# Kernel tuning notes

Hardware: AMD Instinct MI355X
Metric: run time of the kernel (lower is better)

Reference implementation:

```python
import jax, jax.numpy as jnp
import numpy as np

N, E, B, M = 50000, 100000, 50, 50
NPG = N // B            # atoms per graph
DIN, H1, H2, DE, AAF, G = 32, 32, 64, 16, 95, 128
K, T = 3, 6             # ARMA num_stacks, num_layers
F1, F2, F3 = 64, 32, 16
EA = 2 * (M - 1)        # amino-acid edges per graph


def setup_inputs() -> dict:
    key = jax.random.key(0)
    ks = jax.random.split(key, 24)
    s = 0.05
    def w(k, shape):
        return jax.random.normal(k, shape, jnp.float32) * s
    return {
        "x": jax.random.normal(ks[0], (N, DIN), jnp.float32),
        "edge_attr": jax.random.normal(ks[1], (E, DE), jnp.float32),
        "aa_features": jax.random.normal(ks[2], (B, M, AAF), jnp.float32),
        "edge_index": jax.random.randint(ks[3], (2, E), 0, N),
        "monomer_labels": jax.random.randint(ks[4], (B, NPG), 0, M),
        "amino_edge_index": jax.random.randint(ks[5], (2, EA), 0, M),
        "W_e1": w(ks[6], (DE, DIN * H1)), "b_e1": jnp.zeros((DIN * H1,), jnp.float32),
        "root1": w(ks[7], (DIN, H1)), "bias1": jnp.zeros((H1,), jnp.float32),
        "W_e2": w(ks[8], (DE, H1 * H2)), "b_e2": jnp.zeros((H1 * H2,), jnp.float32),
        "root2": w(ks[9], (H1, H2)), "bias2": jnp.zeros((H2,), jnp.float32),
        "Wa_atom": w(ks[10], (H2, 1)), "ba_atom": jnp.zeros((1,), jnp.float32),
        "arma_init_w": w(ks[11], (K, H2 + AAF, G)),
        "arma_w": w(ks[12], (T - 1, K, G, G)),
        "arma_root_w": w(ks[13], (T, K, H2 + AAF, G)),
        "arma_bias": jnp.zeros((T, K, G), jnp.float32),
        "Wa_aa": w(ks[14], (G, 1)), "ba_aa": jnp.zeros((1,), jnp.float32),
        "W1": w(ks[15], (G, F1)), "b1": jnp.zeros((F1,), jnp.float32),
        "W2": w(ks[16], (F1, F2)), "b2": jnp.zeros((F2,), jnp.float32),
        "W3": w(ks[17], (F2, F3)), "b3": jnp.zeros((F3,), jnp.float32),
        "W4": w(ks[18], (F3, 1)), "b4": jnp.zeros((1,), jnp.float32),
    }


def _nnconv(h, src, dst, edge_attr, Wm, bm, root, bias, fin, fout):
    # NNConv (aggr='add'): edge MLP -> per-edge weight matrix, gather-matmul-scatter
    w_e = (edge_attr @ Wm + bm).reshape(-1, fin, fout)            # [E, fin, fout]
    msg = jnp.einsum('ef,efo->eo', h[src], w_e)                   # [E, fout]
    agg = jax.ops.segment_sum(msg, dst, num_segments=h.shape[0])  # scatter-add to targets
    return agg + h @ root + bias


def _forward(x, edge_attr, aa_features, W_e1, b_e1, root1, bias1, W_e2, b_e2, root2, bias2,
             Wa_atom, ba_atom, arma_init_w, arma_w, arma_root_w, arma_bias, Wa_aa, ba_aa,
             W1, b1, W2, b2, W3, b3, W4, b4, edge_index, monomer_labels, amino_edge_index):
    src, dst = edge_index[0], edge_index[1]
    h = jax.nn.relu(_nnconv(x, src, dst, edge_attr, W_e1, b_e1, root1, bias1, DIN, H1))
    h = jax.nn.relu(_nnconv(h, src, dst, edge_attr, W_e2, b_e2, root2, bias2, H1, H2))

    # per-graph attention readout over atoms -> amino-acid embeddings (scatter by monomer label)
    xg = h.reshape(B, NPG, H2)
    attn = jax.nn.softmax(xg @ Wa_atom + ba_atom, axis=1)         # softmax over atoms in graph
    wx = xg * attn
    aa = jax.vmap(lambda wxi, lbl: jax.ops.segment_sum(wxi, lbl, num_segments=M))(wx, monomer_labels)
    h_aa = jnp.concatenate([aa, aa_features], axis=-1)            # [B, M, H2+95]

    # ARMAConv: gcn_norm without self-loops on amino-acid graph (shared across graphs)
    asrc, adst = amino_edge_index[0], amino_edge_index[1]
    deg = jax.ops.segment_sum(jnp.ones((EA,), x.dtype), adst, num_segments=M)
    dinv = jnp.where(deg > 0, 1.0 / jnp.sqrt(jnp.maximum(deg, 1.0)), 0.0)
    norm = dinv[asrc] * dinv[adst]                                # [EA]

    def arma(x0):  # x0: [M, H2+95]
        out = jnp.einsum('mf,kfo->kmo', x0, arma_init_w)          # [K, M, G]
        for t in range(T):
            if t > 0:
                out = jnp.einsum('kmo,kop->kmp', out, arma_w[t - 1])
            msg = out[:, asrc] * norm[None, :, None]              # [K, EA, G]
            prop = jax.vmap(lambda m: jax.ops.segment_sum(m, adst, num_segments=M))(msg)
            rootc = jnp.einsum('mf,kfo->kmo', x0, arma_root_w[t])
            out = jax.nn.relu(prop + rootc + arma_bias[t][:, None, :])
        return out.mean(axis=0)                                   # mean over stacks -> [M, G]

    g = jax.vmap(arma)(h_aa)                                      # [B, M, G]

    # attention readout over amino acids
    attn2 = jax.nn.softmax(g @ Wa_aa + ba_aa, axis=1)
    p = jnp.sum(g * attn2, axis=1)                                # [B, G]

    p = jax.nn.relu(p @ W1 + b1)
    p = jax.nn.relu(p @ W2 + b2)
    p = jax.nn.relu(p @ W3 + b3)
    p = p @ W4 + b4
    return p.reshape(-1)                                          # [B]


def reference(x, edge_attr, aa_features, edge_index, monomer_labels, amino_edge_index,
              W_e1, b_e1, root1, bias1, W_e2, b_e2, root2, bias2, Wa_atom, ba_atom,
              arma_init_w, arma_w, arma_root_w, arma_bias, Wa_aa, ba_aa,
              W1, b1, W2, b2, W3, b3, W4, b4):
    return _forward(x, edge_attr, aa_features, W_e1, b_e1, root1, bias1, W_e2, b_e2, root2, bias2,
                    Wa_atom, ba_atom, arma_init_w, arma_w, arma_root_w, arma_bias, Wa_aa, ba_aa,
                    W1, b1, W2, b2, W3, b3, W4, b4, edge_index, monomer_labels, amino_edge_index)
```

## Files before the change

kernel.cpp:

```cpp
#include <hip/hip_runtime.h>
#include <math.h>

#define N_ATOMS 50000
#define E_EDGES 100000
#define B_G     50
#define M_M     50
#define NPG     1000
#define DIN     32
#define H1C     32
#define H2C     64
#define DEC     16
#define AAF     95
#define G_DIM   128
#define K_ST    3
#define T_L     6
#define EA_E    98
#define XDIM    159
#define NS      21
#define MPAD    64
#define GP      132
#define GPS     136
#define KP2     168
#define KW      544
#define SLC     10
#define APB     100
#define NSB     ((N_ATOMS + 255) / 256)

#define OFF_WE2 (H1C * KW)
#define OFF_WT  (OFF_WE2 + H2C * KW)
#define OFF_AW  (OFF_WT + NS * XDIM * G_DIM)
#define OFF_DEG (OFF_AW + (T_L - 1) * K_ST * G_DIM * G_DIM)
#define PREP_TOTAL (OFF_DEG + E_EDGES)

typedef __attribute__((ext_vector_type(8))) short bf16x8;
typedef __attribute__((ext_vector_type(4))) float f32x4;
typedef __attribute__((ext_vector_type(4))) unsigned int u32x4;

__device__ __forceinline__ short f2bf(float f) {
    unsigned int u = __float_as_uint(f);
    unsigned int r = (u + 0x7FFFu + ((u >> 16) & 1u)) >> 16;
    return (short)r;
}
__device__ __forceinline__ float bf2f(short b) {
    return __uint_as_float(((unsigned int)(unsigned short)b) << 16);
}
__device__ __forceinline__ unsigned int cvtpk_bf16(float lo, float hi) {
    unsigned int r;
    asm("v_cvt_pk_bf16_f32 %0, %1, %2" : "=v"(r) : "v"(lo), "v"(hi));
    return r;
}

__device__ __forceinline__ void f4fma(float4& d, float s, const float4& v) {
    d.x += s * v.x; d.y += s * v.y; d.z += s * v.z; d.w += s * v.w;
}
__device__ __forceinline__ void f4add(float4& d, const float4& v) {
    d.x += v.x; d.y += v.y; d.z += v.z; d.w += v.w;
}
__device__ __forceinline__ void f4relu(float4& d) {
    d.x = fmaxf(d.x, 0.f); d.y = fmaxf(d.y, 0.f);
    d.z = fmaxf(d.z, 0.f); d.w = fmaxf(d.w, 0.f);
}

__global__ __launch_bounds__(256) void prep_all(
    const float* __restrict__ We1, const float* __restrict__ be1, short* __restrict__ WB1,
    const float* __restrict__ We2, const float* __restrict__ be2, short* __restrict__ WB2,
    const float* __restrict__ init_w, const float* __restrict__ root_w, short* __restrict__ Wtb,
    const float* __restrict__ arma_w, short* __restrict__ Wab,
    const int* __restrict__ eidx, int* __restrict__ deg,
    const int* __restrict__ aei, int* __restrict__ aa_off,
    int* __restrict__ aa_src, float* __restrict__ aa_nrm)
{
    int tid = threadIdx.x;
    if (blockIdx.x == 0) {
        __shared__ int   sdeg[M_M];
        __shared__ int   scur[M_M];
        __shared__ float sdinv[M_M];
        __shared__ int   soff[M_M + 1];
        if (tid < M_M) { sdeg[tid] = 0; scur[tid] = 0; }
        __syncthreads();
        if (tid < EA_E) atomicAdd(&sdeg[aei[EA_E + tid]], 1);
        __syncthreads();
        if (tid < M_M) {
            float dv = (float)sdeg[tid];
            sdinv[tid] = (dv > 0.f) ? (1.f / sqrtf(fmaxf(dv, 1.f))) : 0.f;
        }
        __syncthreads();
        if (tid == 0) {
            soff[0] = 0;
            for (int m = 0; m < M_M; ++m) soff[m + 1] = soff[m] + sdeg[m];
        }
        __syncthreads();
        if (tid < EA_E) {
            int ss = aei[tid], dd = aei[EA_E + tid];
            int pos = atomicAdd(&scur[dd], 1);
            int idx = soff[dd] + pos;
            aa_src[idx] = ss;
            aa_nrm[idx] = sdinv[ss] * sdinv[dd];
        }
        if (tid < M_M + 1) aa_off[tid] = soff[tid];
        return;
    }
    int idx = (blockIdx.x - 1) * 256 + tid;
    if (idx < OFF_WE2) {
        int o = idx / KW, k = idx - o * KW;
        float v = (k < 512) ? We1[(size_t)k * H1C + o]
                            : be1[(size_t)(k - 512) * H1C + o];
        WB1[idx] = f2bf(v);
    } else if (idx < OFF_WT) {
        int rem = idx - OFF_WE2;
        int o = rem / KW, k = rem - o * KW;
        float v = (k < 512) ? We2[(size_t)k * H2C + o]
                            : be2[(size_t)(k - 512) * H2C + o];
        WB2[rem] = f2bf(v);
    } else if (idx < OFF_AW) {
        int rem = idx - OFF_WT;
        int s = rem / (XDIM * G_DIM);
        int r2 = rem - s * XDIM * G_DIM;
        int k = r2 / G_DIM, n = r2 - k * G_DIM;
        float v = (s < K_ST) ? init_w[rem]
                             : root_w[(size_t)(s - K_ST) * XDIM * G_DIM + r2];
        Wtb[(size_t)s * G_DIM * KP2 + n * KP2 + k] = f2bf(v);
    } else if (idx < OFF_DEG) {
        int rem = idx - OFF_AW;
        int slot = rem / (G_DIM * G_DIM);
        int r2 = rem - slot * G_DIM * G_DIM;
        int p = r2 / G_DIM, n = r2 - p * G_DIM;
        Wab[(size_t)slot * G_DIM * G_DIM + n * G_DIM + p] = f2bf(arma_w[rem]);
    } else if (idx < PREP_TOTAL) {
        int e = idx - OFF_DEG;
        atomicAdd(&deg[eidx[E_EDGES + e]], 1);
    }
}

__global__ __launch_bounds__(256) void scan_part(const int* __restrict__ deg,
                                                 int* __restrict__ bsum)
{
    __shared__ int tmp[256];
    int tid = threadIdx.x;
    int n = blockIdx.x * 256 + tid;
    tmp[tid] = (n < N_ATOMS) ? deg[n] : 0;
    __syncthreads();
    for (int off = 128; off > 0; off >>= 1) {
        if (tid < off) tmp[tid] += tmp[tid + off];
        __syncthreads();
    }
    if (tid == 0) bsum[blockIdx.x] = tmp[0];
}

__global__ __launch_bounds__(256) void scan_mid(const int* __restrict__ bsum,
                                                int* __restrict__ bpre)
{
    __shared__ int tmp[256];
    int tid = threadIdx.x;
    int v = (tid < NSB) ? bsum[tid] : 0;
    tmp[tid] = v;
    __syncthreads();
    for (int off = 1; off < 256; off <<= 1) {
        int t = tmp[tid];
        int add = (tid >= off) ? tmp[tid - off] : 0;
        __syncthreads();
        tmp[tid] = t + add;
        __syncthreads();
    }
    if (tid < NSB) bpre[tid] = tmp[tid] - v;
}

__global__ __launch_bounds__(256) void scan_out(int* __restrict__ deg_off,
                                                const int* __restrict__ bpre)
{
    __shared__ int tmp[256];
    int tid = threadIdx.x;
    int n = blockIdx.x * 256 + tid;
    int v = (n < N_ATOMS) ? deg_off[n] : 0;
    tmp[tid] = v;
    __syncthreads();
    for (int off = 1; off < 256; off <<= 1) {
        int t = tmp[tid];
        int add = (tid >= off) ? tmp[tid - off] : 0;
        __syncthreads();
        tmp[tid] = t + add;
        __syncthreads();
    }
    int incl = tmp[tid];
    int base = bpre[blockIdx.x];
    if (n < N_ATOMS) deg_off[n] = base + incl - v;
    if (n == N_ATOMS - 1) deg_off[N_ATOMS] = base + incl;
}

template<int FOUT, int NTT, int WGRP, int MTB, bool CIPOS>
__global__ __launch_bounds__(256) void edge_msg_v2(
    const float* __restrict__ h, const float* __restrict__ ea,
    const int* __restrict__ eidx, int* __restrict__ ipos,
    const int* __restrict__ off, int* __restrict__ cursor,
    const short* __restrict__ WB, float* __restrict__ msg)
{
    constexpr int KS = 17;
    __shared__ int iplds[MTB * 16];
    int tid  = threadIdx.x;
    int lane = tid & 63, wave = tid >> 6;
    int l16  = lane & 15, quad = lane >> 4;
    int nt   = wave % NTT, tg = wave / NTT;
    int ebase = blockIdx.x * (MTB * 16);

    if (CIPOS) {
        if (tid < MTB * 16) {
            int e = ebase + tid;
            if (e < E_EDGES) {
                int d = eidx[E_EDGES + e];
                int pos = atomicAdd(&cursor[d], 1);
                int p = off[d] + pos;
                iplds[tid] = p;
                ipos[e] = p;
            }
        }
    }

    bf16x8 Bfr[KS];
    {
        const short* wb = WB + (size_t)(nt * 16 + l16) * KW;
        #pragma unroll
        for (int ks = 0; ks < KS; ++ks)
            Bfr[ks] = *(const bf16x8*)(wb + ks * 32 + quad * 8);
    }
    if (CIPOS) __syncthreads();

    for (int t = tg; t < MTB; t += WGRP) {
        int e  = ebase + t * 16 + l16;
        int es = (e < E_EDGES) ? e : (E_EDGES - 1);
        int s  = eidx[es];
        float4 h0 = *(const float4*)(h + (size_t)s * 32 + quad * 8);
        float4 h1 = *(const float4*)(h + (size_t)s * 32 + quad * 8 + 4);
        float hf[8] = {h0.x, h0.y, h0.z, h0.w, h1.x, h1.y, h1.z, h1.w};
        float4 e0 = *(const float4*)(ea + (size_t)es * DEC);
        float4 e1 = *(const float4*)(ea + (size_t)es * DEC + 4);
        float4 e2 = *(const float4*)(ea + (size_t)es * DEC + 8);
        float4 e3 = *(const float4*)(ea + (size_t)es * DEC + 12);
        float eaf[16] = {e0.x, e0.y, e0.z, e0.w, e1.x, e1.y, e1.z, e1.w,
                         e2.x, e2.y, e2.z, e2.w, e3.x, e3.y, e3.z, e3.w};

        f32x4 acc = (f32x4){0.f, 0.f, 0.f, 0.f};
        #pragma unroll
        for (int ks = 0; ks < KS; ++ks) {
            u32x4 av;
            if (ks < DEC) {
                float fac = eaf[ks];
                #pragma unroll
                for (int j = 0; j < 4; ++j)
                    av[j] = cvtpk_bf16(fac * hf[2 * j], fac * hf[2 * j + 1]);
            } else {
                #pragma unroll
                for (int j = 0; j < 4; ++j)
                    av[j] = cvtpk_bf16(hf[2 * j], hf[2 * j + 1]);
            }
            bf16x8 a = __builtin_bit_cast(bf16x8, av);
            acc = __builtin_amdgcn_mfma_f32_16x16x32_bf16(a, Bfr[ks], acc, 0, 0, 0);
        }
        int erb = ebase + t * 16 + quad * 4;
        #pragma unroll
        for (int r = 0; r < 4; ++r) {
            int ee = erb + r;
            if (ee < E_EDGES) {
                int p = CIPOS ? iplds[t * 16 + quad * 4 + r] : ipos[ee];
                msg[(size_t)p * FOUT + nt * 16 + l16] = acc[r];
            }
        }
    }
}

template<int FIN, int FOUT, bool SCORE>
__global__ __launch_bounds__(256) void gather_update(
    const float* __restrict__ msg, const int* __restrict__ off,
    const float* __restrict__ hin,
    const float* __restrict__ root, const float* __restrict__ bias,
    float* __restrict__ hout,
    const float* __restrict__ wa, const float* __restrict__ ba,
    float* __restrict__ sc)
{
    constexpr int NPB = 256 / FOUT;
    __shared__ float rlds[FIN][FOUT];
    __shared__ float hlds[NPB][FIN];
    int tid = threadIdx.x;
    for (int i = tid; i < FIN * FOUT / 4; i += 256) {
        *(float4*)&rlds[0][i * 4] = *(const float4*)(root + i * 4);
    }
    int nb = blockIdx.x * NPB;
    for (int i = tid; i < NPB * FIN; i += 256) {
        int ln = i / FIN, f = i % FIN;
        int n = nb + ln;
        hlds[ln][f] = (n < N_ATOMS) ? hin[(size_t)n * FIN + f] : 0.f;
    }
    __syncthreads();

    int ln = tid / FOUT, o = tid % FOUT;
    int n = nb + ln;
    if (n >= N_ATOMS) return;
    float acc = bias[o];
    #pragma unroll 8
    for (int f = 0; f < FIN; ++f) acc += hlds[ln][f] * rlds[f][o];
    int j0 = off[n], j1 = off[n + 1];
    for (int j = j0; j < j1; ++j) {
        acc += msg[(size_t)j * FOUT + o];
    }
    float hv = fmaxf(acc, 0.f);
    hout[(size_t)n * FOUT + o] = hv;
    if constexpr (SCORE) {
        static_assert(FOUT == 64, "score fusion needs node==wave");
        float sv = hv * wa[o];
        #pragma unroll
        for (int d = 32; d > 0; d >>= 1) sv += __shfl_down(sv, d);
        if (o == 0) sc[n] = sv + ba[0];
    }
}

__global__ __launch_bounds__(256) void atom_scatter_sm(
    const float* __restrict__ h2, const float* __restrict__ sc,
    const int* __restrict__ labels, float* __restrict__ partial)
{
    __shared__ float aa4[4][M_M][H2C];
    __shared__ float red[256];
    int b = blockIdx.x / SLC, s = blockIdx.x % SLC;
    int tid = threadIdx.x;
    int wave = tid >> 6, lane = tid & 63;
    const float* sb = sc + (size_t)b * NPG;

    for (int i = tid; i < 4 * M_M * H2C; i += 256) ((float*)aa4)[i] = 0.f;

    float lmax = -1e30f;
    for (int n = tid; n < NPG; n += 256) lmax = fmaxf(lmax, sb[n]);
    red[tid] = lmax;
    __syncthreads();
    for (int off = 128; off > 0; off >>= 1) {
        if (tid < off) red[tid] = fmaxf(red[tid], red[tid + off]);
        __syncthreads();
    }
    float mx = red[0];
    __syncthreads();
    float lsum = 0.f;
    for (int n = tid; n < NPG; n += 256) lsum += expf(sb[n] - mx);
    red[tid] = lsum;
    __syncthreads();
    for (int off = 128; off > 0; off >>= 1) {
        if (tid < off) red[tid] += red[tid + off];
        __syncthreads();
    }
    float inv = 1.f / red[0];
    __syncthreads();

    int nbase = s * APB;
    const float* hb = h2 + (size_t)b * NPG * H2C;
    #pragma unroll 5
    for (int it = 0; it < APB / 4; ++it) {
        int n = nbase + it * 4 + wave;
        int lbl = labels[b * NPG + n];
        float w = expf(sb[n] - mx) * inv;
        float hv = hb[(size_t)n * H2C + lane];
        aa4[wave][lbl][lane] += hv * w;
    }
    __syncthreads();
    float* pb = partial + (size_t)(b * SLC + s) * M_M * H2C;
    for (int i = tid; i < M_M * H2C; i += 256) {
        float v = ((float*)aa4)[i] + ((float*)aa4)[M_M * H2C + i]
                + ((float*)aa4)[2 * M_M * H2C + i] + ((float*)aa4)[3 * M_M * H2C + i];
        pb[i] = v;
    }
}

__global__ __launch_bounds__(256) void x0_finalize(
    const float* __restrict__ partial, const float* __restrict__ aaf,
    short* __restrict__ x0b)
{
    int idx = blockIdx.x * 256 + threadIdx.x;
    if (idx >= B_G * MPAD * KP2) return;
    int b = idx / (MPAD * KP2);
    int rem = idx - b * (MPAD * KP2);
    int m = rem / KP2, k = rem - m * KP2;
    float v = 0.f;
    if (m < M_M) {
        if (k < H2C) {
            const float* pb = partial + (size_t)b * SLC * M_M * H2C + m * H2C + k;
            #pragma unroll
            for (int s = 0; s < SLC; ++s) v += pb[(size_t)s * (M_M * H2C)];
        } else if (k < XDIM) {
            v = aaf[((size_t)b * M_M + m) * AAF + (k - H2C)];
        }
    }
    x0b[idx] = f2bf(v);
}

__global__ __launch_bounds__(256) void rc_gemm_mfma(
    const short* __restrict__ x0b, const short* __restrict__ Wtb,
    float* __restrict__ RC)
{
    int b = blockIdx.x / NS, s = blockIdx.x % NS;
    int tid = threadIdx.x;
    int lane = tid & 63, wave = tid >> 6;
    int l16 = lane & 15, quad = lane >> 4;
    const short* xa = x0b + (size_t)b * MPAD * KP2 + (wave * 16 + l16) * KP2;
    const short* wb = Wtb + (size_t)s * G_DIM * KP2;

    f32x4 acc[8];
    #pragma unroll
    for (int nt = 0; nt < 8; ++nt) acc[nt] = (f32x4){0.f, 0.f, 0.f, 0.f};

    #pragma unroll
    for (int ks = 0; ks < 5; ++ks) {
        bf16x8 a = *(const bf16x8*)(xa + ks * 32 + quad * 8);
        #pragma unroll
        for (int nt = 0; nt < 8; ++nt) {
            bf16x8 bf = *(const bf16x8*)(wb + (nt * 16 + l16) * KP2 + ks * 32 + quad * 8);
            acc[nt] = __builtin_amdgcn_mfma_f32_16x16x32_bf16(a, bf, acc[nt], 0, 0, 0);
        }
    }
    float* op = RC + (size_t)(b * NS + s) * M_M * G_DIM;
    #pragma unroll
    for (int nt = 0; nt < 8; ++nt) {
        #pragma unroll
        for (int r = 0; r < 4; ++r) {
            int m = wave * 16 + quad * 4 + r;
            if (m < M_M)
                op[m * G_DIM + nt * 16 + l16] = acc[nt][r];
        }
    }
}

__global__ __launch_bounds__(512) void arma_iter(
    const float* __restrict__ RC, const short* __restrict__ Wab,
    const float* __restrict__ arma_bias,
    const int* __restrict__ aa_off, const int* __restrict__ aa_src,
    const float* __restrict__ aa_nrm, float* __restrict__ gfull)
{
    __shared__ float Abuf[MPAD][GP];
    __shared__ float Bbuf[MPAD][GP];
    __shared__ short Bb16[MPAD][GPS];
    __shared__ int   s_off[M_M + 1];
    __shared__ int   s_src[EA_E];
    __shared__ float s_nrm[EA_E];
    int b = blockIdx.x / K_ST, k = blockIdx.x % K_ST;
    int tid = threadIdx.x;
    int oi = tid & 15, mi = tid >> 4;
    int c0 = oi * 4, c1 = 64 + oi * 4;
    int lane = tid & 63, wave = tid >> 6;
    int l16 = lane & 15, quad = lane >> 4;
    int mt = wave >> 1, nh = wave & 1;

    const float* rcb = RC + (size_t)b * NS * M_M * G_DIM;
    if (tid < M_M + 1) s_off[tid] = aa_off[tid];
    if (tid < EA_E) { s_src[tid] = aa_src[tid]; s_nrm[tid] = aa_nrm[tid]; }

    for (int i = tid; i < MPAD * G_DIM; i += 512) {
        int m = i >> 7, o = i & 127;
        Abuf[m][o] = (m < M_M) ? rcb[(size_t)k * M_M * G_DIM + i] : 0.f;
    }
    for (int i = tid; i < MPAD * GPS / 2; i += 512) {
        ((int*)Bb16)[i] = 0;
    }
    __syncthreads();

    for (int t = 0; t < T_L; ++t) {
        if (t > 0) {
            const short* aw = Wab + (size_t)((t - 1) * K_ST + k) * G_DIM * G_DIM;
            f32x4 acc[4];
            #pragma unroll
            for (int nt = 0; nt < 4; ++nt) acc[nt] = (f32x4){0.f, 0.f, 0.f, 0.f};
            #pragma unroll
            for (int ks = 0; ks < 4; ++ks) {
                bf16x8 a = *(const bf16x8*)&Bb16[mt * 16 + l16][ks * 32 + quad * 8];
                #pragma unroll
                for (int nt = 0; nt < 4; ++nt) {
                    int n0 = (nh * 4 + nt) * 16 + l16;
                    bf16x8 bf = *(const bf16x8*)(aw + n0 * G_DIM + ks * 32 + quad * 8);
                    acc[nt] = __builtin_amdgcn_mfma_f32_16x16x32_bf16(a, bf, acc[nt], 0, 0, 0);
                }
            }
            #pragma unroll
            for (int nt = 0; nt < 4; ++nt) {
                #pragma unroll
                for (int r = 0; r < 4; ++r) {
                    Abuf[mt * 16 + quad * 4 + r][(nh * 4 + nt) * 16 + l16] = acc[nt][r];
                }
            }
            __syncthreads();
        }
        const float* rct = rcb + (size_t)(K_ST + t * K_ST + k) * M_M * G_DIM;
        const float* bb  = arma_bias + ((size_t)t * K_ST + k) * G_DIM;
        float4 bias0 = *(const float4*)(bb + c0);
        float4 bias1 = *(const float4*)(bb + c1);
        #pragma unroll
        for (int r = 0; r < 2; ++r) {
            int m = mi * 2 + r;
            if (m < M_M) {
                const float* rr = rct + (size_t)m * G_DIM;
                float4 v0 = bias0, v1 = bias1;
                f4add(v0, *(const float4*)(rr + c0));
                f4add(v1, *(const float4*)(rr + c1));
                int j0 = s_off[m], j1 = s_off[m + 1];
                for (int j = j0; j < j1; ++j) {
                    float nv = s_nrm[j];
                    const float* ap = &Abuf[s_src[j]][0];
                    f4fma(v0, nv, *(const float4*)(ap + c0));
                    f4fma(v1, nv, *(const float4*)(ap + c1));
                }
                f4relu(v0);
                f4relu(v1);
                *(float4*)&Bbuf[m][c0] = v0;
                *(float4*)&Bbuf[m][c1] = v1;
                unsigned int p0 = cvtpk_bf16(v0.x, v0.y);
                unsigned int p1 = cvtpk_bf16(v0.z, v0.w);
                unsigned int p2 = cvtpk_bf16(v1.x, v1.y);
                unsigned int p3 = cvtpk_bf16(v1.z, v1.w);
                *(uint2*)&Bb16[m][c0] = make_uint2(p0, p1);
                *(uint2*)&Bb16[m][c1] = make_uint2(p2, p3);
            }
        }
        __syncthreads();
    }
    float* gb = gfull + ((size_t)(b * K_ST + k)) * M_M * G_DIM;
    for (int i = tid; i < M_M * G_DIM; i += 512) {
        int m = i >> 7, o = i & 127;
        gb[i] = Bbuf[m][o];
    }
}

__global__ __launch_bounds__(128) void aa_readout_mlp(
    const float* __restrict__ gfull, const float* __restrict__ wa,
    const float* __restrict__ ba,
    const float* __restrict__ W1, const float* __restrict__ b1,
    const float* __restrict__ W2, const float* __restrict__ b2,
    const float* __restrict__ W3, const float* __restrict__ b3,
    const float* __restrict__ W4, const float* __restrict__ b4,
    float* __restrict__ out)
{
    __shared__ float g[M_M][G_DIM + 1];
    __shared__ float s2[M_M];
    __shared__ float p[G_DIM];
    __shared__ float r1[64], r2[32], r3[16];
    int b = blockIdx.x, tid = threadIdx.x;
    const float* g0 = gfull + (size_t)b * K_ST * M_M * G_DIM;
    for (int i = tid; i < M_M * G_DIM; i += 128) {
        int m = i >> 7, o = i & 127;
        g[m][o] = (g0[i] + g0[M_M*G_DIM + i] + g0[2*M_M*G_DIM + i]) * (1.f/3.f);
    }
    __syncthreads();
    if (tid < M_M) {
        float sv = ba[0];
        for (int o = 0; o < G_DIM; ++o) sv += g[tid][o] * wa[o];
        s2[tid] = sv;
    }
    __syncthreads();
    if (tid == 0) {
        float mx = -1e30f;
        for (int m = 0; m < M_M; ++m) mx = fmaxf(mx, s2[m]);
        float den = 0.f;
        for (int m = 0; m < M_M; ++m) den += expf(s2[m] - mx);
        float inv = 1.f / den;
        for (int m = 0; m < M_M; ++m) s2[m] = expf(s2[m] - mx) * inv;
    }
    __syncthreads();
    {
        float pv = 0.f;
        for (int m = 0; m < M_M; ++m) pv += g[m][tid] * s2[m];
        p[tid] = pv;
    }
    __syncthreads();
    if (tid < 64) {
        float v = b1[tid];
        for (int i = 0; i < 128; ++i) v += p[i] * W1[i * 64 + tid];
        r1[tid] = fmaxf(v, 0.f);
    }
    __syncthreads();
    if (tid < 32) {
        float v = b2[tid];
        for (int i = 0; i < 64; ++i) v += r1[i] * W2[i * 32 + tid];
        r2[tid] = fmaxf(v, 0.f);
    }
    __syncthreads();
    if (tid < 16) {
        float v = b3[tid];
        for (int i = 0; i < 32; ++i) v += r2[i] * W3[i * 16 + tid];
        r3[tid] = fmaxf(v, 0.f);
    }
    __syncthreads();
    if (tid == 0) {
        float v = b4[0];
        for (int i = 0; i < 16; ++i) v += r3[i] * W4[i];
        out[b] = v;
    }
}

extern "C" void kernel_launch(void* const* d_in, const int* in_sizes, int n_in,
                              void* d_out, int out_size, void* d_ws, size_t ws_size,
                              hipStream_t stream)
{
    (void)in_sizes; (void)n_in; (void)out_size; (void)ws_size;
    const float* x            = (const float*)d_in[0];
    const float* edge_attr    = (const float*)d_in[1];
    const float* aa_features  = (const float*)d_in[2];
    const int*   edge_index   = (const int*)  d_in[3];
    const int*   mono_labels  = (const int*)  d_in[4];
    const int*   amino_ei     = (const int*)  d_in[5];
    const float* W_e1 = (const float*)d_in[6];
    const float* b_e1 = (const float*)d_in[7];
    const float* root1= (const float*)d_in[8];
    const float* bias1= (const float*)d_in[9];
    const float* W_e2 = (const float*)d_in[10];
    const float* b_e2 = (const float*)d_in[11];
    const float* root2= (const float*)d_in[12];
    const float* bias2= (const float*)d_in[13];
    const float* Wa_atom = (const float*)d_in[14];
    const float* ba_atom = (const float*)d_in[15];
    const float* arma_init_w = (const float*)d_in[16];
    const float* arma_w      = (const float*)d_in[17];
    const float* arma_root_w = (const float*)d_in[18];
    const float* arma_bias   = (const float*)d_in[19];
    const float* Wa_aa = (const float*)d_in[20];
    const float* ba_aa = (const float*)d_in[21];
    const float* W1 = (const float*)d_in[22];
    const float* b1 = (const float*)d_in[23];
    const float* W2 = (const float*)d_in[24];
    const float* b2 = (const float*)d_in[25];
    const float* W3 = (const float*)d_in[26];
    const float* b3 = (const float*)d_in[27];
    const float* W4 = (const float*)d_in[28];
    const float* b4 = (const float*)d_in[29];

    float* ws = (float*)d_ws;
    float* h1    = ws;
    float* h2    = h1   + (size_t)N_ATOMS * H1C;
    float* h_aa  = h2   + (size_t)N_ATOMS * H2C;
    float* sc    = h_aa + (size_t)B_G * M_M * XDIM;
    int*   aa_off = (int*)(sc + (size_t)B_G * NPG);
    int*   aa_src = aa_off + (M_M + 1);
    float* aa_nrm = (float*)(aa_src + EA_E);
    int*   deg_off = (int*)(aa_nrm + EA_E);
    int*   cursor  = deg_off + (N_ATOMS + 1);
    int*   ipos    = cursor + N_ATOMS;
    int*   bsum    = ipos + E_EDGES;
    int*   bpre    = bsum + 256;
    float* RC    = (float*)(bpre + 256);
    float* gfull = RC + (size_t)B_G * NS * M_M * G_DIM;
    short* Wtb   = (short*)((((uintptr_t)(gfull + (size_t)B_G * K_ST * M_M * G_DIM)) + 15)
                            & ~(uintptr_t)15);
    short* x0b   = Wtb + (size_t)NS * G_DIM * KP2;
    short* Wab   = x0b + (size_t)B_G * MPAD * KP2;
    short* WB1   = Wab + (size_t)(T_L - 1) * K_ST * G_DIM * G_DIM;
    short* WB2   = WB1 + (size_t)H1C * KW;
    float* msg   = RC;
    float* partial = RC;
    (void)h_aa;

    (void)hipMemsetAsync(deg_off, 0, (2 * N_ATOMS + 1) * sizeof(int), stream);

    prep_all<<<1 + (PREP_TOTAL + 255) / 256, 256, 0, stream>>>(
        W_e1, b_e1, WB1, W_e2, b_e2, WB2,
        arma_init_w, arma_root_w, Wtb, arma_w, Wab,
        edge_index, deg_off, amino_ei, aa_off, aa_src, aa_nrm);

    scan_part<<<NSB, 256, 0, stream>>>(deg_off, bsum);
    scan_mid<<<1, 256, 0, stream>>>(bsum, bpre);
    scan_out<<<NSB, 256, 0, stream>>>(deg_off, bpre);

    edge_msg_v2<H1C, 2, 2, 8, true><<<(E_EDGES + 127) / 128, 256, 0, stream>>>(
        x, edge_attr, edge_index, ipos, deg_off, cursor, WB1, msg);
    gather_update<DIN, H1C, false><<<(N_ATOMS + 7) / 8, 256, 0, stream>>>(
        msg, deg_off, x, root1, bias1, h1, nullptr, nullptr, nullptr);
    edge_msg_v2<H2C, 4, 1, 4, false><<<(E_EDGES + 63) / 64, 256, 0, stream>>>(
        h1, edge_attr, edge_index, ipos, nullptr, nullptr, WB2, msg);
    gather_update<H1C, H2C, true><<<(N_ATOMS + 3) / 4, 256, 0, stream>>>(
        msg, deg_off, h1, root2, bias2, h2, Wa_atom, ba_atom, sc);

    atom_scatter_sm<<<B_G * SLC, 256, 0, stream>>>(h2, sc, mono_labels, partial);
    x0_finalize<<<(B_G * MPAD * KP2 + 255) / 256, 256, 0, stream>>>(
        partial, aa_features, x0b);

    rc_gemm_mfma<<<B_G * NS, 256, 0, stream>>>(x0b, Wtb, RC);
    arma_iter<<<B_G * K_ST, 512, 0, stream>>>(RC, Wab, arma_bias,
                                              aa_off, aa_src, aa_nrm, gfull);
    aa_readout_mlp<<<B_G, 128, 0, stream>>>(gfull, Wa_aa, ba_aa, W1, b1, W2, b2, W3, b3, W4, b4,
                                            (float*)d_out);
}
```

Measured before the change: 315.2 us.

## Fuse root GEMM into ARMA kernel, single-block scan, larger edge tile

Replaces the three-kernel degree prefix scan with one 1024-thread single-block scan. It also removes the separate rc_gemm_mfma kernel and its global RC intermediate by computing the x0 root/init products inside arma_iter with MFMA, keeping A fragments in registers and writing to a new shared Rbuf. The second edge message kernel now handles 8 tiles per block instead of 4. This saves launches and global traffic in exchange for more shared memory per block and redundant per-stack weight reads inside arma_iter.

Measured after the change: 396.0 us. +25.6%, slower.

```diff
diff --git a/kernel.cpp b/kernel.cpp
--- a/kernel.cpp
+++ b/kernel.cpp
@@ -24,7 +24,6 @@
 #define KW      544
 #define SLC     10
 #define APB     100
-#define NSB     ((N_ATOMS + 255) / 256)
 
 #define OFF_WE2 (H1C * KW)
 #define OFF_WT  (OFF_WE2 + H2C * KW)
@@ -132,59 +131,36 @@
     }
 }
 
-__global__ __launch_bounds__(256) void scan_part(const int* __restrict__ deg,
-                                                 int* __restrict__ bsum)
-{
-    __shared__ int tmp[256];
+#define SCHUNK ((N_ATOMS + 1023) / 1024)
+
+__global__ __launch_bounds__(1024) void scan_all(int* __restrict__ deg_off)
+{
+    __shared__ int psum[1024];
     int tid = threadIdx.x;
-    int n = blockIdx.x * 256 + tid;
-    tmp[tid] = (n < N_ATOMS) ? deg[n] : 0;
-    __syncthreads();
-    for (int off = 128; off > 0; off >>= 1) {
-        if (tid < off) tmp[tid] += tmp[tid + off];
-        __syncthreads();
-    }
-    if (tid == 0) bsum[blockIdx.x] = tmp[0];
-}
-
-__global__ __launch_bounds__(256) void scan_mid(const int* __restrict__ bsum,
-                                                int* __restrict__ bpre)
-{
-    __shared__ int tmp[256];
-    int tid = threadIdx.x;
-    int v = (tid < NSB) ? bsum[tid] : 0;
-    tmp[tid] = v;
-    __syncthreads();
-    for (int off = 1; off < 256; off <<= 1) {
-        int t = tmp[tid];
-        int add = (tid >= off) ? tmp[tid - off] : 0;
-        __syncthreads();
-        tmp[tid] = t + add;
-        __syncthreads();
-    }
-    if (tid < NSB) bpre[tid] = tmp[tid] - v;
-}
-
-__global__ __launch_bounds__(256) void scan_out(int* __restrict__ deg_off,
-                                                const int* __restrict__ bpre)
-{
-    __shared__ int tmp[256];
-    int tid = threadIdx.x;
-    int n = blockIdx.x * 256 + tid;
-    int v = (n < N_ATOMS) ? deg_off[n] : 0;
-    tmp[tid] = v;
-    __syncthreads();
-    for (int off = 1; off < 256; off <<= 1) {
-        int t = tmp[tid];
-        int add = (tid >= off) ? tmp[tid - off] : 0;
-        __syncthreads();
-        tmp[tid] = t + add;
-        __syncthreads();
-    }
-    int incl = tmp[tid];
-    int base = bpre[blockIdx.x];
-    if (n < N_ATOMS) deg_off[n] = base + incl - v;
-    if (n == N_ATOMS - 1) deg_off[N_ATOMS] = base + incl;
+    int base = tid * SCHUNK;
+    int s = 0;
+    for (int i = 0; i < SCHUNK; ++i) {
+        int n = base + i;
+        if (n < N_ATOMS) s += deg_off[n];
+    }
+    psum[tid] = s;
+    __syncthreads();
+    for (int off = 1; off < 1024; off <<= 1) {
+        int t = psum[tid];
+        int add = (tid >= off) ? psum[tid - off] : 0;
+        __syncthreads();
+        psum[tid] = t + add;
+        __syncthreads();
+    }
+    int run = (tid > 0) ? psum[tid - 1] : 0;
+    for (int i = 0; i < SCHUNK; ++i) {
+        int n = base + i;
+        if (n <= N_ATOMS) {
+            int v = (n < N_ATOMS) ? deg_off[n] : 0;
+            deg_off[n] = run;
+            run += v;
+        }
+    }
 }
 
 template<int FOUT, int NTT, int WGRP, int MTB, bool CIPOS>
@@ -387,50 +363,15 @@
     x0b[idx] = f2bf(v);
 }
 
-__global__ __launch_bounds__(256) void rc_gemm_mfma(
+__global__ __launch_bounds__(512) void arma_iter(
     const short* __restrict__ x0b, const short* __restrict__ Wtb,
-    float* __restrict__ RC)
-{
-    int b = blockIdx.x / NS, s = blockIdx.x % NS;
-    int tid = threadIdx.x;
-    int lane = tid & 63, wave = tid >> 6;
-    int l16 = lane & 15, quad = lane >> 4;
-    const short* xa = x0b + (size_t)b * MPAD * KP2 + (wave * 16 + l16) * KP2;
-    const short* wb = Wtb + (size_t)s * G_DIM * KP2;
-
-    f32x4 acc[8];
-    #pragma unroll
-    for (int nt = 0; nt < 8; ++nt) acc[nt] = (f32x4){0.f, 0.f, 0.f, 0.f};
-
-    #pragma unroll
-    for (int ks = 0; ks < 5; ++ks) {
-        bf16x8 a = *(const bf16x8*)(xa + ks * 32 + quad * 8);
-        #pragma unroll
-        for (int nt = 0; nt < 8; ++nt) {
-            bf16x8 bf = *(const bf16x8*)(wb + (nt * 16 + l16) * KP2 + ks * 32 + quad * 8);
-            acc[nt] = __builtin_amdgcn_mfma_f32_16x16x32_bf16(a, bf, acc[nt], 0, 0, 0);
-        }
-    }
-    float* op = RC + (size_t)(b * NS + s) * M_M * G_DIM;
-    #pragma unroll
-    for (int nt = 0; nt < 8; ++nt) {
-        #pragma unroll
-        for (int r = 0; r < 4; ++r) {
-            int m = wave * 16 + quad * 4 + r;
-            if (m < M_M)
-                op[m * G_DIM + nt * 16 + l16] = acc[nt][r];
-        }
-    }
-}
-
-__global__ __launch_bounds__(512) void arma_iter(
-    const float* __restrict__ RC, const short* __restrict__ Wab,
-    const float* __restrict__ arma_bias,
+    const short* __restrict__ Wab, const float* __restrict__ arma_bias,
     const int* __restrict__ aa_off, const int* __restrict__ aa_src,
     const float* __restrict__ aa_nrm, float* __restrict__ gfull)
 {
     __shared__ float Abuf[MPAD][GP];
     __shared__ float Bbuf[MPAD][GP];
+    __shared__ float Rbuf[MPAD][GP];
     __shared__ short Bb16[MPAD][GPS];
     __shared__ int   s_off[M_M + 1];
     __shared__ int   s_src[EA_E];
@@ -443,18 +384,43 @@
     int l16 = lane & 15, quad = lane >> 4;
     int mt = wave >> 1, nh = wave & 1;
 
-    const float* rcb = RC + (size_t)b * NS * M_M * G_DIM;
     if (tid < M_M + 1) s_off[tid] = aa_off[tid];
     if (tid < EA_E) { s_src[tid] = aa_src[tid]; s_nrm[tid] = aa_nrm[tid]; }
-
-    for (int i = tid; i < MPAD * G_DIM; i += 512) {
-        int m = i >> 7, o = i & 127;
-        Abuf[m][o] = (m < M_M) ? rcb[(size_t)k * M_M * G_DIM + i] : 0.f;
-    }
     for (int i = tid; i < MPAD * GPS / 2; i += 512) {
         ((int*)Bb16)[i] = 0;
     }
-    __syncthreads();
+
+    bf16x8 Afr[5];
+    {
+        const short* xb = x0b + (size_t)b * MPAD * KP2 + (mt * 16 + l16) * KP2;
+        #pragma unroll
+        for (int ks = 0; ks < 5; ++ks)
+            Afr[ks] = *(const bf16x8*)(xb + ks * 32 + quad * 8);
+    }
+
+    auto x0_gemm = [&](const short* __restrict__ W, float (*dst)[GP]) {
+        f32x4 acc[4];
+        #pragma unroll
+        for (int nt = 0; nt < 4; ++nt) acc[nt] = (f32x4){0.f, 0.f, 0.f, 0.f};
+        #pragma unroll
+        for (int ks = 0; ks < 5; ++ks) {
+            #pragma unroll
+            for (int nt = 0; nt < 4; ++nt) {
+                int n0 = (nh * 4 + nt) * 16 + l16;
+                bf16x8 bf = *(const bf16x8*)(W + (size_t)n0 * KP2 + ks * 32 + quad * 8);
+                acc[nt] = __builtin_amdgcn_mfma_f32_16x16x32_bf16(Afr[ks], bf, acc[nt], 0, 0, 0);
+            }
+        }
+        #pragma unroll
+        for (int nt = 0; nt < 4; ++nt) {
+            #pragma unroll
+            for (int r = 0; r < 4; ++r) {
+                dst[mt * 16 + quad * 4 + r][(nh * 4 + nt) * 16 + l16] = acc[nt][r];
+            }
+        }
+    };
+
+    x0_gemm(Wtb + (size_t)k * G_DIM * KP2, Abuf);
 
     for (int t = 0; t < T_L; ++t) {
         if (t > 0) {
@@ -479,20 +445,20 @@
                     Abuf[mt * 16 + quad * 4 + r][(nh * 4 + nt) * 16 + l16] = acc[nt][r];
                 }
             }
-            __syncthreads();
-        }
-        const float* rct = rcb + (size_t)(K_ST + t * K_ST + k) * M_M * G_DIM;
-        const float* bb  = arma_bias + ((size_t)t * K_ST + k) * G_DIM;
+        }
+        x0_gemm(Wtb + (size_t)(K_ST + t * K_ST + k) * G_DIM * KP2, Rbuf);
+        __syncthreads();
+
+        const float* bb = arma_bias + ((size_t)t * K_ST + k) * G_DIM;
         float4 bias0 = *(const float4*)(bb + c0);
         float4 bias1 = *(const float4*)(bb + c1);
         #pragma unroll
         for (int r = 0; r < 2; ++r) {
             int m = mi * 2 + r;
             if (m < M_M) {
-                const float* rr = rct + (size_t)m * G_DIM;
                 float4 v0 = bias0, v1 = bias1;
-                f4add(v0, *(const float4*)(rr + c0));
-                f4add(v1, *(const float4*)(rr + c1));
+                f4add(v0, *(const float4*)&Rbuf[m][c0]);
+                f4add(v1, *(const float4*)&Rbuf[m][c1]);
                 int j0 = s_off[m], j1 = s_off[m + 1];
                 for (int j = j0; j < j1; ++j) {
                     float nv = s_nrm[j];
@@ -655,15 +621,13 @@
         arma_init_w, arma_root_w, Wtb, arma_w, Wab,
         edge_index, deg_off, amino_ei, aa_off, aa_src, aa_nrm);
 
-    scan_part<<<NSB, 256, 0, stream>>>(deg_off, bsum);
-    scan_mid<<<1, 256, 0, stream>>>(bsum, bpre);
-    scan_out<<<NSB, 256, 0, stream>>>(deg_off, bpre);
+    scan_all<<<1, 1024, 0, stream>>>(deg_off);
 
     edge_msg_v2<H1C, 2, 2, 8, true><<<(E_EDGES + 127) / 128, 256, 0, stream>>>(
         x, edge_attr, edge_index, ipos, deg_off, cursor, WB1, msg);
     gather_update<DIN, H1C, false><<<(N_ATOMS + 7) / 8, 256, 0, stream>>>(
         msg, deg_off, x, root1, bias1, h1, nullptr, nullptr, nullptr);
-    edge_msg_v2<H2C, 4, 1, 4, false><<<(E_EDGES + 63) / 64, 256, 0, stream>>>(
+    edge_msg_v2<H2C, 4, 1, 8, false><<<(E_EDGES + 127) / 128, 256, 0, stream>>>(
         h1, edge_attr, edge_index, ipos, nullptr, nullptr, WB2, msg);
     gather_update<H1C, H2C, true><<<(N_ATOMS + 3) / 4, 256, 0, stream>>>(
         msg, deg_off, h1, root2, bias2, h2, Wa_atom, ba_atom, sc);
@@ -672,8 +636,7 @@
     x0_finalize<<<(B_G * MPAD * KP2 + 255) / 256, 256, 0, stream>>>(
         partial, aa_features, x0b);
 
-    rc_gemm_mfma<<<B_G * NS, 256, 0, stream>>>(x0b, Wtb, RC);
-    arma_iter<<<B_G * K_ST, 512, 0, stream>>>(RC, Wab, arma_bias,
+    arma_iter<<<B_G * K_ST, 512, 0, stream>>>(x0b, Wtb, Wab, arma_bias,
                                               aa_off, aa_src, aa_nrm, gfull);
     aa_readout_mlp<<<B_G, 128, 0, stream>>>(gfull, Wa_aa, ba_aa, W1, b1, W2, b2, W3, b3, W4, b4,
                                             (float*)d_out);
```
